# Optimization experiments

Measured on AMD Instinct MI355X. Metric: run time of the kernel, lower is better.

Reference implementation:

```python
import jax, jax.numpy as jnp
import numpy as np

PAD = 0
LS = 0.1          # label smoothing
END_W = 3.0       # end_weight
CHAR_W = 0.2      # char_weight
LEN_P = 0.3       # length_penalty
DIFF_MULT = 1.0   # difficulty 'easy'


def _position_weight_matrix(S):
    # Row L-1 holds the position weights for a sequence of length L,
    # replicating the Python loop in get_position_weights.
    Lf = jnp.arange(1, S + 1, dtype=jnp.float32)[:, None]   # [S,1] length
    jf = jnp.arange(S, dtype=jnp.float32)[None, :]           # [1,S] position
    Li = jnp.arange(1, S + 1)[:, None]
    ji = jnp.arange(S)[None, :]
    valid = ji < Li
    w = jnp.where(valid, 1.0 + (jf / Lf) * 0.5, 1.0)
    w = jnp.where(ji == Li - 1, END_W * 1.5, w)               # last char
    w = jnp.where((Li >= 2) & (ji == Li - 2), END_W * 1.0, w)
    w = jnp.where((Li >= 3) & (ji == Li - 3), END_W * 0.8, w)
    mid = (Li >= 4) & (ji >= Li // 3) & (ji < (2 * Li) // 3)
    w = jnp.where(mid, w * 1.3, w)
    w = jnp.where((Li <= 4) & valid, w * 1.2, w)              # short seqs
    return w


def setup_inputs() -> dict:
    key = jax.random.key(0)
    k1, k2 = jax.random.split(key)
    output = jax.random.normal(k1, (512, 128, 2048), dtype=jnp.float32)
    target = jax.random.randint(k2, (512, 128), 0, 2048)
    return {"output": output, "target": target}


def reference(output, target):
    B, S, V = output.shape
    f32 = jnp.float32
    pad_mask = target != PAD
    lens = pad_mask.sum(axis=1)                                # [B]

    # --- label-smoothed CE, ignore_index=PAD, reduction='none' ---
    logp = jax.nn.log_softmax(output, axis=-1)                 # [B,S,V]
    nll = -jnp.take_along_axis(logp, target[..., None], axis=-1)[..., 0]
    ce = (1.0 - LS) * nll + LS * (-logp.mean(axis=-1))
    ce = jnp.where(pad_mask, ce, 0.0)                          # [B,S]

    # --- position-weighted CE ---
    W = _position_weight_matrix(S)                             # [S,S]
    rows = W[jnp.clip(lens - 1, 0, S - 1)]                     # [B,S]
    pos = jnp.arange(S)[None, :]
    bw = jnp.where(pos < lens[:, None], rows, 1.0)             # [B,S]
    weighted_loss = (ce * bw).sum() / bw.sum()

    # --- length penalty ---
    preds = jnp.argmax(output, axis=-1)                        # [B,S]
    plen = (preds != PAD).sum(axis=1)
    diff = jnp.abs(plen.astype(f32) - lens.astype(f32))
    factor = 1.0 + 0.5 * (plen < lens).astype(f32) + 0.3 * (plen <= 3).astype(f32)
    length_pen = LEN_P * (diff * factor).mean()

    # --- n-gram one-hot MSE, computed analytically (exact, no [B,S,V] one-hots):
    # per position the bigram/trigram one-hots have at most one nonzero, so
    # sum_v (p*w - t*w)^2 = w^2 * (exists_p + exists_t - 2*match).
    pb = preds[:, :-1] == preds[:, 1:]                         # pred bigram exists
    tb = target[:, :-1] == target[:, 1:]
    mb = pb & tb & (preds[:, :-1] == target[:, :-1])
    bwts = jnp.where(jnp.arange(S - 1) >= S - 3, 1.5, 1.0)     # last two = 1.5
    bcnt = pb.astype(f32) + tb.astype(f32) - 2.0 * mb.astype(f32)
    bigram_loss = (bcnt * (bwts ** 2)).sum() / (B * (S - 1) * V)

    pt = pb[:, :-1] & pb[:, 1:]                                # pred trigram exists
    tt = tb[:, :-1] & tb[:, 1:]
    mt = pt & tt & (preds[:, :-2] == target[:, :-2])
    twts = jnp.where(jnp.arange(S - 2) >= S - 4, 2.0, 1.0)     # last two = 2.0
    tcnt = pt.astype(f32) + tt.astype(f32) - 2.0 * mt.astype(f32)
    trigram_loss = (tcnt * (twts ** 2)).sum() / (B * (S - 2) * V)
    any_valid = jnp.any(pad_mask[:, :-2].sum(axis=1) > 0)
    ngram_loss = bigram_loss + jnp.where(any_valid, 1.5 * trigram_loss, 0.0)

    total = DIFF_MULT * (weighted_loss * 0.7 + length_pen * 0.2 + CHAR_W * ngram_loss * 0.1)
    return total
```

## Files before the change

kernel.cpp:

```cpp
#include <hip/hip_runtime.h>
#include <math.h>

#define BB 512
#define SS 128
#define VV 2048
#define NROWS (BB * SS)

constexpr float LSc    = 0.1f;
constexpr float END_W  = 3.0f;
constexpr float CHAR_W = 0.2f;
constexpr float LEN_P  = 0.3f;

typedef float f4 __attribute__((ext_vector_type(4)));

__global__ __launch_bounds__(256) void k_rows(const float* __restrict__ x,
                                              const int* __restrict__ tgt,
                                              float* __restrict__ ce,
                                              int* __restrict__ preds,
                                              float* __restrict__ acc,
                                              int* __restrict__ flagcnt) {
    if (blockIdx.x == 0 && threadIdx.x == 0) {
        for (int i = 0; i < 5; ++i) acc[i] = 0.f;
        flagcnt[0] = 0;
        flagcnt[1] = 0;
    }

    const int lane = threadIdx.x & 63;
    const int row  = blockIdx.x * 4 + (threadIdx.x >> 6);
    const float* rp = x + (size_t)row * VV;
    const int t  = tgt[row];
    const float xt = rp[t];

    const f4* rp4 = (const f4*)rp;
    f4 v[8];
#pragma unroll
    for (int k = 0; k < 8; ++k)
        v[k] = __builtin_nontemporal_load(rp4 + k * 64 + lane);

    float m = v[0].x; int mi = lane * 4;
    float ssum = 0.f, esum = 0.f;
#pragma unroll
    for (int k = 0; k < 8; ++k) {
        const int base = k * 256 + lane * 4;
        const float f0 = v[k].x, f1 = v[k].y, f2 = v[k].z, f3 = v[k].w;
        ssum += (f0 + f1) + (f2 + f3);
        esum += (__expf(f0) + __expf(f1)) + (__expf(f2) + __expf(f3));
        if (f0 > m) { m = f0; mi = base;     }
        if (f1 > m) { m = f1; mi = base + 1; }
        if (f2 > m) { m = f2; mi = base + 2; }
        if (f3 > m) { m = f3; mi = base + 3; }
    }

#pragma unroll
    for (int off = 1; off < 64; off <<= 1) {
        float om = __shfl_xor(m,    off);
        int   oi = __shfl_xor(mi,   off);
        float os = __shfl_xor(ssum, off);
        float oe = __shfl_xor(esum, off);
        ssum += os;
        esum += oe;
        if (om > m || (om == m && oi < mi)) { m = om; mi = oi; }
    }

    if (lane == 0) {
        float lse = logf(esum);
        float nll = lse - xt;
        float cev = (1.0f - LSc) * nll + LSc * (lse - ssum * (1.0f / VV));
        ce[row]    = (t != 0) ? cev : 0.0f;
        preds[row] = mi;
    }
}

__global__ __launch_bounds__(128) void k_batch(const int* __restrict__ tgt,
                                               const int* __restrict__ preds,
                                               const float* __restrict__ ce,
                                               float* __restrict__ acc,
                                               int* __restrict__ flagcnt,
                                               float* __restrict__ out) {
    const int b = blockIdx.x;
    const int j = threadIdx.x;

    __shared__ int   st[SS];
    __shared__ int   sp[SS];
    __shared__ int   ired[128];
    __shared__ float fred[128][4];

    int   t = tgt[b * SS + j];
    int   p = preds[b * SS + j];
    float c = ce[b * SS + j];
    st[j] = t; sp[j] = p;

    ired[j] = (t != 0 ? 1 : 0) | ((p != 0 ? 1 : 0) << 8)
            | (((t != 0 && j < SS - 2) ? 1 : 0) << 16);
    __syncthreads();
    for (int off = 64; off >= 1; off >>= 1) {
        if (j < off) ired[j] += ired[j + off];
        __syncthreads();
    }
    const int r  = ired[0];
    const int L  = r & 255;
    const int P  = (r >> 8) & 255;
    const int VC = r >> 16;

    float w = 1.0f;
    if (L > 0 && j < L) {
        w = 1.0f + 0.5f * ((float)j / (float)L);
        if (j == L - 1)                w = END_W * 1.5f;
        else if (L >= 2 && j == L - 2) w = END_W * 1.0f;
        else if (L >= 3 && j == L - 3) w = END_W * 0.8f;
        if (L >= 4 && j >= L / 3 && j < (2 * L) / 3) w *= 1.3f;
        if (L <= 4) w *= 1.2f;
    }

    float big = 0.f, tri = 0.f;
    if (j < SS - 1) {
        bool pb = sp[j] == sp[j + 1];
        bool tb = st[j] == st[j + 1];
        bool mb = pb && tb && (sp[j] == st[j]);
        float wt = (j >= SS - 3) ? 2.25f : 1.0f;
        big = ((pb ? 1.f : 0.f) + (tb ? 1.f : 0.f) - 2.f * (mb ? 1.f : 0.f)) * wt;
    }
    if (j < SS - 2) {
        bool pt = (sp[j] == sp[j + 1]) && (sp[j + 1] == sp[j + 2]);
        bool tt = (st[j] == st[j + 1]) && (st[j + 1] == st[j + 2]);
        bool mt = pt && tt && (sp[j] == st[j]);
        float wt = (j >= SS - 4) ? 4.0f : 1.0f;
        tri = ((pt ? 1.f : 0.f) + (tt ? 1.f : 0.f) - 2.f * (mt ? 1.f : 0.f)) * wt;
    }

    fred[j][0] = c * w;
    fred[j][1] = w;
    fred[j][2] = big;
    fred[j][3] = tri;
    __syncthreads();
    for (int off = 64; off >= 1; off >>= 1) {
        if (j < off) {
            fred[j][0] += fred[j + off][0];
            fred[j][1] += fred[j + off][1];
            fred[j][2] += fred[j + off][2];
            fred[j][3] += fred[j + off][3];
        }
        __syncthreads();
    }
    if (j == 0) {
        atomicAdd(&acc[0], fred[0][0]);
        atomicAdd(&acc[1], fred[0][1]);
        float diff   = fabsf((float)P - (float)L);
        float factor = 1.0f + (P < L ? 0.5f : 0.f) + (P <= 3 ? 0.3f : 0.f);
        atomicAdd(&acc[2], diff * factor);
        atomicAdd(&acc[3], fred[0][2]);
        atomicAdd(&acc[4], fred[0][3]);
        if (VC > 0) atomicOr(&flagcnt[0], 1);

        __threadfence();
        int old = __hip_atomic_fetch_add(&flagcnt[1], 1, __ATOMIC_ACQ_REL,
                                         __HIP_MEMORY_SCOPE_AGENT);
        if (old == BB - 1) {
            float a0 = __hip_atomic_load(&acc[0], __ATOMIC_RELAXED, __HIP_MEMORY_SCOPE_AGENT);
            float a1 = __hip_atomic_load(&acc[1], __ATOMIC_RELAXED, __HIP_MEMORY_SCOPE_AGENT);
            float a2 = __hip_atomic_load(&acc[2], __ATOMIC_RELAXED, __HIP_MEMORY_SCOPE_AGENT);
            float a3 = __hip_atomic_load(&acc[3], __ATOMIC_RELAXED, __HIP_MEMORY_SCOPE_AGENT);
            float a4 = __hip_atomic_load(&acc[4], __ATOMIC_RELAXED, __HIP_MEMORY_SCOPE_AGENT);
            int   fl = __hip_atomic_load(&flagcnt[0], __ATOMIC_RELAXED, __HIP_MEMORY_SCOPE_AGENT);
            float wl = a0 / a1;
            float lp = LEN_P * a2 * (1.0f / BB);
            float bg = a3 / (float)(BB * (SS - 1) * VV);
            float tg = a4 / (float)(BB * (SS - 2) * VV);
            float ng = bg + (fl ? 1.5f * tg : 0.f);
            out[0] = wl * 0.7f + lp * 0.2f + CHAR_W * ng * 0.1f;
        }
    }
}

extern "C" void kernel_launch(void* const* d_in, const int* in_sizes, int n_in,
                              void* d_out, int out_size, void* d_ws, size_t ws_size,
                              hipStream_t stream) {
    const float* x   = (const float*)d_in[0];
    const int*   tgt = (const int*)d_in[1];
    float*       out = (float*)d_out;

    float* ce      = (float*)d_ws;
    int*   preds   = (int*)((char*)d_ws + (size_t)NROWS * 4);
    float* acc     = (float*)((char*)d_ws + (size_t)2 * NROWS * 4);
    int*   flagcnt = (int*)(acc + 5);

    k_rows<<<NROWS / 4, 256, 0, stream>>>(x, tgt, ce, preds, acc, flagcnt);
    k_batch<<<BB, 128, 0, stream>>>(tgt, preds, ce, acc, flagcnt, out);
}
```

Measured before the change: 140.0 us.

## Process two rows per wave, extract target logit from registers, shuffle reductions

Each wave now loads two full vocab rows up front (16 vector loads in flight) and processes both, halving the grid. The target logit is picked from the already-loaded registers via a lane shuffle instead of a separate dependent global load. The per-lane argmax uses four independent chains, and nontemporal loads are replaced with regular loads. The batch kernel's shared-memory tree reductions are replaced by wave shuffles plus a two-entry combine. In exchange, register pressure per thread doubles, which may reduce occupancy.

Result: slower. 155.7 us (+11.2%).

```diff
diff --git a/kernel.cpp b/kernel.cpp
--- a/kernel.cpp
+++ b/kernel.cpp
@@ -12,6 +12,63 @@
 constexpr float LEN_P  = 0.3f;
 
 typedef float f4 __attribute__((ext_vector_type(4)));
+
+__device__ __forceinline__ void process_row(const f4 v[8], int row, int t,
+                                            float* __restrict__ ce,
+                                            int* __restrict__ preds) {
+    const int lane  = threadIdx.x & 63;
+    const int lane4 = lane * 4;
+
+    float m0 = v[0].x, m1 = v[0].y, m2 = v[0].z, m3 = v[0].w;
+    int   i0 = 0,      i1 = 0,      i2 = 0,      i3 = 0;
+#pragma unroll
+    for (int k = 1; k < 8; ++k) {
+        if (v[k].x > m0) { m0 = v[k].x; i0 = k; }
+        if (v[k].y > m1) { m1 = v[k].y; i1 = k; }
+        if (v[k].z > m2) { m2 = v[k].z; i2 = k; }
+        if (v[k].w > m3) { m3 = v[k].w; i3 = k; }
+    }
+    float m = m0; int mi = i0 * 256 + lane4;
+    { int c = i1 * 256 + lane4 + 1; if (m1 > m || (m1 == m && c < mi)) { m = m1; mi = c; } }
+    { int c = i2 * 256 + lane4 + 2; if (m2 > m || (m2 == m && c < mi)) { m = m2; mi = c; } }
+    { int c = i3 * 256 + lane4 + 3; if (m3 > m || (m3 == m && c < mi)) { m = m3; mi = c; } }
+
+    float s0 = 0, s1 = 0, s2 = 0, s3 = 0;
+    float e0 = 0, e1 = 0, e2 = 0, e3 = 0;
+#pragma unroll
+    for (int k = 0; k < 8; ++k) {
+        s0 += v[k].x;         s1 += v[k].y;
+        s2 += v[k].z;         s3 += v[k].w;
+        e0 += __expf(v[k].x); e1 += __expf(v[k].y);
+        e2 += __expf(v[k].z); e3 += __expf(v[k].w);
+    }
+    float ssum = (s0 + s1) + (s2 + s3);
+    float esum = (e0 + e1) + (e2 + e3);
+
+#pragma unroll
+    for (int off = 1; off < 64; off <<= 1) {
+        float om = __shfl_xor(m,  off);
+        int   oi = __shfl_xor(mi, off);
+        ssum += __shfl_xor(ssum, off);
+        esum += __shfl_xor(esum, off);
+        if (om > m || (om == m && oi < mi)) { m = om; mi = oi; }
+    }
+
+    const int kt = t >> 8, lt = (t >> 2) & 63, jt = t & 3;
+    f4 sel = v[0];
+#pragma unroll
+    for (int k = 1; k < 8; ++k) if (kt == k) sel = v[k];
+    float comp = (jt == 0) ? sel.x : (jt == 1) ? sel.y : (jt == 2) ? sel.z : sel.w;
+    float xt = __shfl(comp, lt);
+
+    if (lane == 0) {
+        float lse = logf(esum);
+        float nll = lse - xt;
+        float cev = (1.0f - LSc) * nll + LSc * (lse - ssum * (1.0f / VV));
+        ce[row]    = (t != 0) ? cev : 0.0f;
+        preds[row] = mi;
+    }
+}
 
 __global__ __launch_bounds__(256) void k_rows(const float* __restrict__ x,
                                               const int* __restrict__ tgt,
@@ -26,49 +83,24 @@
     }
 
     const int lane = threadIdx.x & 63;
-    const int row  = blockIdx.x * 4 + (threadIdx.x >> 6);
-    const float* rp = x + (size_t)row * VV;
-    const int t  = tgt[row];
-    const float xt = rp[t];
-
-    const f4* rp4 = (const f4*)rp;
-    f4 v[8];
-#pragma unroll
-    for (int k = 0; k < 8; ++k)
-        v[k] = __builtin_nontemporal_load(rp4 + k * 64 + lane);
-
-    float m = v[0].x; int mi = lane * 4;
-    float ssum = 0.f, esum = 0.f;
-#pragma unroll
-    for (int k = 0; k < 8; ++k) {
-        const int base = k * 256 + lane * 4;
-        const float f0 = v[k].x, f1 = v[k].y, f2 = v[k].z, f3 = v[k].w;
-        ssum += (f0 + f1) + (f2 + f3);
-        esum += (__expf(f0) + __expf(f1)) + (__expf(f2) + __expf(f3));
-        if (f0 > m) { m = f0; mi = base;     }
-        if (f1 > m) { m = f1; mi = base + 1; }
-        if (f2 > m) { m = f2; mi = base + 2; }
-        if (f3 > m) { m = f3; mi = base + 3; }
-    }
-
-#pragma unroll
-    for (int off = 1; off < 64; off <<= 1) {
-        float om = __shfl_xor(m,    off);
-        int   oi = __shfl_xor(mi,   off);
-        float os = __shfl_xor(ssum, off);
-        float oe = __shfl_xor(esum, off);
-        ssum += os;
-        esum += oe;
-        if (om > m || (om == m && oi < mi)) { m = om; mi = oi; }
-    }
-
-    if (lane == 0) {
-        float lse = logf(esum);
-        float nll = lse - xt;
-        float cev = (1.0f - LSc) * nll + LSc * (lse - ssum * (1.0f / VV));
-        ce[row]    = (t != 0) ? cev : 0.0f;
-        preds[row] = mi;
-    }
+    const int wid  = blockIdx.x * 4 + (threadIdx.x >> 6);
+    const int rowA = wid * 2;
+    const int rowB = rowA + 1;
+
+    const f4* pA = (const f4*)(x + (size_t)rowA * VV);
+    const f4* pB = (const f4*)(x + (size_t)rowB * VV);
+
+    f4 a[8], b[8];
+#pragma unroll
+    for (int k = 0; k < 8; ++k) a[k] = pA[k * 64 + lane];
+#pragma unroll
+    for (int k = 0; k < 8; ++k) b[k] = pB[k * 64 + lane];
+
+    const int tA = tgt[rowA];
+    const int tB = tgt[rowB];
+
+    process_row(a, rowA, tA, ce, preds);
+    process_row(b, rowB, tB, ce, preds);
 }
 
 __global__ __launch_bounds__(128) void k_batch(const int* __restrict__ tgt,
@@ -77,39 +109,41 @@
                                                float* __restrict__ acc,
                                                int* __restrict__ flagcnt,
                                                float* __restrict__ out) {
-    const int b = blockIdx.x;
-    const int j = threadIdx.x;
+    const int b    = blockIdx.x;
+    const int j    = threadIdx.x;
+    const int lane = j & 63;
+    const int w    = j >> 6;
 
     __shared__ int   st[SS];
     __shared__ int   sp[SS];
-    __shared__ int   ired[128];
-    __shared__ float fred[128][4];
+    __shared__ int   xi[2];
+    __shared__ float xf[2][4];
 
     int   t = tgt[b * SS + j];
     int   p = preds[b * SS + j];
     float c = ce[b * SS + j];
     st[j] = t; sp[j] = p;
 
-    ired[j] = (t != 0 ? 1 : 0) | ((p != 0 ? 1 : 0) << 8)
-            | (((t != 0 && j < SS - 2) ? 1 : 0) << 16);
+    int packed = (t != 0 ? 1 : 0) | ((p != 0 ? 1 : 0) << 8)
+               | (((t != 0 && j < SS - 2) ? 1 : 0) << 16);
+#pragma unroll
+    for (int off = 1; off < 64; off <<= 1) packed += __shfl_xor(packed, off);
+    if (lane == 0) xi[w] = packed;
     __syncthreads();
-    for (int off = 64; off >= 1; off >>= 1) {
-        if (j < off) ired[j] += ired[j + off];
-        __syncthreads();
-    }
-    const int r  = ired[0];
+
+    const int r  = xi[0] + xi[1];
     const int L  = r & 255;
     const int P  = (r >> 8) & 255;
     const int VC = r >> 16;
 
-    float w = 1.0f;
+    float wgt = 1.0f;
     if (L > 0 && j < L) {
-        w = 1.0f + 0.5f * ((float)j / (float)L);
-        if (j == L - 1)                w = END_W * 1.5f;
-        else if (L >= 2 && j == L - 2) w = END_W * 1.0f;
-        else if (L >= 3 && j == L - 3) w = END_W * 0.8f;
-        if (L >= 4 && j >= L / 3 && j < (2 * L) / 3) w *= 1.3f;
-        if (L <= 4) w *= 1.2f;
+        wgt = 1.0f + 0.5f * ((float)j / (float)L);
+        if (j == L - 1)                wgt = END_W * 1.5f;
+        else if (L >= 2 && j == L - 2) wgt = END_W * 1.0f;
+        else if (L >= 3 && j == L - 3) wgt = END_W * 0.8f;
+        if (L >= 4 && j >= L / 3 && j < (2 * L) / 3) wgt *= 1.3f;
+        if (L <= 4) wgt *= 1.2f;
     }
 
     float big = 0.f, tri = 0.f;
@@ -128,28 +162,25 @@
         tri = ((pt ? 1.f : 0.f) + (tt ? 1.f : 0.f) - 2.f * (mt ? 1.f : 0.f)) * wt;
     }
 
-    fred[j][0] = c * w;
-    fred[j][1] = w;
-    fred[j][2] = big;
-    fred[j][3] = tri;
+    float f0 = c * wgt, f1 = wgt, f2 = big, f3 = tri;
+#pragma unroll
+    for (int off = 1; off < 64; off <<= 1) {
+        f0 += __shfl_xor(f0, off);
+        f1 += __shfl_xor(f1, off);
+        f2 += __shfl_xor(f2, off);
+        f3 += __shfl_xor(f3, off);
+    }
+    if (lane == 0) { xf[w][0] = f0; xf[w][1] = f1; xf[w][2] = f2; xf[w][3] = f3; }
     __syncthreads();
-    for (int off = 64; off >= 1; off >>= 1) {
-        if (j < off) {
-            fred[j][0] += fred[j + off][0];
-            fred[j][1] += fred[j + off][1];
-            fred[j][2] += fred[j + off][2];
-            fred[j][3] += fred[j + off][3];
-        }
-        __syncthreads();
-    }
+
     if (j == 0) {
-        atomicAdd(&acc[0], fred[0][0]);
-        atomicAdd(&acc[1], fred[0][1]);
+        atomicAdd(&acc[0], xf[0][0] + xf[1][0]);
+        atomicAdd(&acc[1], xf[0][1] + xf[1][1]);
         float diff   = fabsf((float)P - (float)L);
         float factor = 1.0f + (P < L ? 0.5f : 0.f) + (P <= 3 ? 0.3f : 0.f);
         atomicAdd(&acc[2], diff * factor);
-        atomicAdd(&acc[3], fred[0][2]);
-        atomicAdd(&acc[4], fred[0][3]);
+        atomicAdd(&acc[3], xf[0][2] + xf[1][2]);
+        atomicAdd(&acc[4], xf[0][3] + xf[1][3]);
         if (VC > 0) atomicOr(&flagcnt[0], 1);
 
         __threadfence();
@@ -184,6 +215,6 @@
     float* acc     = (float*)((char*)d_ws + (size_t)2 * NROWS * 4);
     int*   flagcnt = (int*)(acc + 5);
 
-    k_rows<<<NROWS / 4, 256, 0, stream>>>(x, tgt, ce, preds, acc, flagcnt);
+    k_rows<<<NROWS / 8, 256, 0, stream>>>(x, tgt, ce, preds, acc, flagcnt);
     k_batch<<<BB, 128, 0, stream>>>(tgt, preds, ce, acc, flagcnt, out);
 }
```
